# Kernel tuning notes

Hardware: AMD Instinct MI355X
Metric: run time of the kernel (lower is better)

Reference implementation:

```python
import jax, jax.numpy as jnp
import numpy as np

EPS = 1e-5
CHUNK = 512


def _bn(x, gamma, beta):
    # BatchNorm1d in training mode: biased batch statistics over the batch dim
    m = x.mean(axis=0)
    v = ((x - m) ** 2).mean(axis=0)
    return (x - m) * jax.lax.rsqrt(v + EPS) * gamma + beta


def _xavier(k, fan_in, fan_out):
    lim = float(np.sqrt(6.0 / (fan_in + fan_out)))
    return jax.random.uniform(k, (fan_in, fan_out), minval=-lim, maxval=lim, dtype=jnp.float32)


def setup_inputs() -> dict:
    key = jax.random.key(0)
    ks = jax.random.split(key, 10)
    B, CH_S, CH_H, T = 8192, 512, 2048, 3
    D = CH_H * T  # 6144 = 12 chunks of 512
    inp = {
        "fs": jax.random.normal(ks[0], (B, CH_S), dtype=jnp.float32),
        "ft0": jax.random.normal(ks[1], (B, CH_H), dtype=jnp.float32),
        "ft1": jax.random.normal(ks[2], (B, CH_H), dtype=jnp.float32),
        "ft2": jax.random.normal(ks[3], (B, CH_H), dtype=jnp.float32),
        # fixed (non-trainable in the original: plain tensor) score key [512, 1]
        "score_key": jax.random.uniform(ks[4], (CHUNK, 1), dtype=jnp.float32),
        # align_t: Linear(D,2048) -> BN -> Linear(2048,2048) -> BN -> Linear(2048,CH_H) -> ReLU
        "W1": _xavier(ks[5], D, 2048), "b1": jnp.zeros((2048,), jnp.float32),
        "g1": jnp.ones((2048,), jnp.float32), "beta1": jnp.zeros((2048,), jnp.float32),
        "W2": _xavier(ks[6], 2048, 2048), "b2": jnp.zeros((2048,), jnp.float32),
        "g2": jnp.ones((2048,), jnp.float32), "beta2": jnp.zeros((2048,), jnp.float32),
        "W3": _xavier(ks[7], 2048, CH_H), "b3": jnp.zeros((CH_H,), jnp.float32),
        # extend: Linear(CH_H, D) -> ReLU
        "We": _xavier(ks[8], CH_H, D), "bE": jnp.zeros((D,), jnp.float32),
    }
    return inp


def reference(fs, ft0, ft1, ft2, score_key, W1, b1, g1, beta1, W2, b2, g2, beta2, W3, b3, We, bE):
    # fs is accepted but unused, mirroring the original forward
    ft_all = jnp.concatenate([ft0, ft1, ft2], axis=1)  # [B, D]
    B, D = ft_all.shape
    n_chunks = D // CHUNK
    chunks = ft_all.reshape(B, n_chunks, CHUNK)  # [B, C, 512]
    # chunked score matmul against key[512,1], softmax over chunks
    score = jax.nn.softmax(jnp.einsum("bck,k->bc", chunks, score_key[:, 0]), axis=1)  # [B, C]
    # per-chunk reweighting: x <- x + x*score  == x*(1+score), one broadcasted multiply
    ft_all = (chunks * (1.0 + score[:, :, None])).reshape(B, D)
    # align_t MLP (BatchNorm in training mode, no activation between first layers)
    h = _bn(ft_all @ W1 + b1, g1, beta1)
    h = _bn(h @ W2 + b2, g2, beta2)
    aligned_t = jax.nn.relu(h @ W3 + b3)
    extend_t = jax.nn.relu(aligned_t @ We + bE)
    return aligned_t, extend_t, ft_all
```

## Files before the change

kernel.cpp:

```cpp
#include <hip/hip_runtime.h>
#include <hip/hip_bf16.h>
#include <cstdint>
#include <cstddef>

using bf16x8 = __attribute__((ext_vector_type(8))) __bf16;
using f32x4  = __attribute__((ext_vector_type(4))) float;

__device__ __forceinline__ unsigned short f2bf(float f) {
  unsigned int u = __float_as_uint(f);
  u += 0x7FFFu + ((u >> 16) & 1u);
  return (unsigned short)(u >> 16);
}

__device__ __forceinline__ void async_cp16(const void* g, void* l) {
  __builtin_amdgcn_global_load_lds(
      (const __attribute__((address_space(1))) unsigned int*)g,
      (__attribute__((address_space(3))) unsigned int*)l, 16, 0, 0);
}

__global__ __launch_bounds__(256) void wconv(const float* __restrict__ W,
                                             unsigned short* __restrict__ Wt,
                                             int K, int N) {
  __shared__ float tile[32][33];
  const int n0 = blockIdx.x * 32;
  const int k0 = blockIdx.y * 32;
  const int tx = threadIdx.x;
  const int ty = threadIdx.y;
  for (int i = 0; i < 32; i += 8)
    tile[ty + i][tx] = W[(size_t)(k0 + ty + i) * N + n0 + tx];
  __syncthreads();
  for (int i = 0; i < 32; i += 8)
    Wt[(size_t)(n0 + ty + i) * K + k0 + tx] = f2bf(tile[tx][ty + i]);
}

__global__ __launch_bounds__(256) void score_kernel(
    const float* __restrict__ ft0, const float* __restrict__ ft1,
    const float* __restrict__ ft2, const float* __restrict__ key,
    float* __restrict__ out_f, unsigned short* __restrict__ out_b) {
  const int row  = blockIdx.x;
  const int t    = threadIdx.x;
  const int lane = t & 63;
  const int w    = t >> 6;
  const int h    = t >> 7;
  __shared__ float wsum[6][4];
  __shared__ float mult[12];

  const float4* k4 = (const float4*)key;
  float4 v[6];
#pragma unroll
  for (int i = 0; i < 6; i++) {
    const int idx4 = t + 256 * i;
    const int e    = idx4 * 4;
    const float* tsrc = (i < 2) ? ft0 : (i < 4) ? ft1 : ft2;
    v[i] = *(const float4*)(tsrc + (size_t)row * 2048 + (e & 2047));
    float4 kv = k4[idx4 & 127];
    float p = v[i].x * kv.x + v[i].y * kv.y + v[i].z * kv.z + v[i].w * kv.w;
#pragma unroll
    for (int o = 32; o > 0; o >>= 1) p += __shfl_down(p, o, 64);
    if (lane == 0) wsum[i][w] = p;
  }
  __syncthreads();
  if (t == 0) {
    float s[12];
    float mx = -1e30f;
    for (int c = 0; c < 12; c++) {
      s[c] = wsum[c >> 1][2 * (c & 1)] + wsum[c >> 1][2 * (c & 1) + 1];
      mx = fmaxf(mx, s[c]);
    }
    float tot = 0.f;
    for (int c = 0; c < 12; c++) { s[c] = expf(s[c] - mx); tot += s[c]; }
    const float inv = 1.0f / tot;
    for (int c = 0; c < 12; c++) mult[c] = 1.0f + s[c] * inv;
  }
  __syncthreads();
#pragma unroll
  for (int i = 0; i < 6; i++) {
    const int idx4 = t + 256 * i;
    const int e    = idx4 * 4;
    const float m  = mult[2 * i + h];
    float4 o;
    o.x = v[i].x * m; o.y = v[i].y * m; o.z = v[i].z * m; o.w = v[i].w * m;
    *(float4*)(out_f + (size_t)row * 6144 + e) = o;
    ushort4 ob;
    ob.x = f2bf(o.x); ob.y = f2bf(o.y); ob.z = f2bf(o.z); ob.w = f2bf(o.w);
    *(ushort4*)(out_b + (size_t)row * 6144 + e) = ob;
  }
}

template <int EPI>
__global__ __launch_bounds__(256, 2) void gemm_kernel(
    const unsigned short* __restrict__ A,
    const unsigned short* __restrict__ Bt,
    const float* __restrict__ bias,
    float* __restrict__ C,
    unsigned short* __restrict__ Cbf,
    int M, int N, int K) {
  __shared__ __align__(16) unsigned short As[128 * 32];
  __shared__ __align__(16) unsigned short Bs[128 * 32];
  const int t    = threadIdx.x;
  const int lane = t & 63;
  const int w    = t >> 6;
  const size_t m0 = (size_t)blockIdx.y * 128;
  const size_t n0 = (size_t)blockIdx.x * 128;
  const int wm   = (w >> 1) * 64;
  const int wn   = (w & 1) * 64;
  const int frow = lane & 15;
  const int quad = lane >> 4;

  const int c0 = w * 128 + lane;
  const int c1 = c0 + 64;
  const unsigned short* gA0 = A  + (m0 + (c0 >> 2)) * (size_t)K + (c0 & 3) * 8;
  const unsigned short* gA1 = A  + (m0 + (c1 >> 2)) * (size_t)K + (c1 & 3) * 8;
  const unsigned short* gB0 = Bt + (n0 + (c0 >> 2)) * (size_t)K + (c0 & 3) * 8;
  const unsigned short* gB1 = Bt + (n0 + (c1 >> 2)) * (size_t)K + (c1 & 3) * 8;
  unsigned short* lA0 = As + (size_t)(w * 128) * 8;
  unsigned short* lA1 = As + (size_t)(w * 128 + 64) * 8;
  unsigned short* lB0 = Bs + (size_t)(w * 128) * 8;
  unsigned short* lB1 = Bs + (size_t)(w * 128 + 64) * 8;

  f32x4 acc[4][4];
  const f32x4 z = {0.f, 0.f, 0.f, 0.f};
#pragma unroll
  for (int i = 0; i < 4; i++)
#pragma unroll
    for (int j = 0; j < 4; j++) acc[i][j] = z;

  for (int k0 = 0; k0 < K; k0 += 32) {
    async_cp16(gA0 + k0, lA0);
    async_cp16(gA1 + k0, lA1);
    async_cp16(gB0 + k0, lB0);
    async_cp16(gB1 + k0, lB1);
    __syncthreads();
    bf16x8 af[4], bfr[4];
#pragma unroll
    for (int i = 0; i < 4; i++)
      af[i] = *(const bf16x8*)(As + (wm + i * 16 + frow) * 32 + quad * 8);
#pragma unroll
    for (int i = 0; i < 4; i++)
      bfr[i] = *(const bf16x8*)(Bs + (wn + i * 16 + frow) * 32 + quad * 8);
#pragma unroll
    for (int mi = 0; mi < 4; mi++)
#pragma unroll
      for (int ni = 0; ni < 4; ni++)
        acc[mi][ni] = __builtin_amdgcn_mfma_f32_16x16x32_bf16(af[mi], bfr[ni], acc[mi][ni], 0, 0, 0);
    __syncthreads();
  }

#pragma unroll
  for (int mi = 0; mi < 4; mi++) {
    const size_t rowb = m0 + wm + mi * 16 + quad * 4;
#pragma unroll
    for (int ni = 0; ni < 4; ni++) {
      const size_t col = n0 + wn + ni * 16 + frow;
      const float bv = bias[col];
#pragma unroll
      for (int r = 0; r < 4; r++) {
        float v = acc[mi][ni][r] + bv;
        if (EPI == 1) v = fmaxf(v, 0.f);
        const size_t idx = (rowb + r) * (size_t)N + col;
        C[idx] = v;
        if (EPI == 1 && Cbf != nullptr) Cbf[idx] = f2bf(v);
      }
    }
  }
}

__global__ __launch_bounds__(256) void bn_accum(const float* __restrict__ h,
                                                float* __restrict__ ps,
                                                float* __restrict__ pq, int N) {
  const int c  = blockIdx.x * 256 + threadIdx.x;
  const int r0 = blockIdx.y * 256;
  const float* p = h + (size_t)r0 * N + c;
  float s = 0.f, q = 0.f;
  for (int r = 0; r < 256; r++) {
    float x = p[(size_t)r * N];
    s += x; q += x * x;
  }
  ps[(size_t)blockIdx.y * N + c] = s;
  pq[(size_t)blockIdx.y * N + c] = q;
}

__global__ __launch_bounds__(256) void bn_final(const float* __restrict__ ps,
                                                const float* __restrict__ pq,
                                                const float* __restrict__ g,
                                                const float* __restrict__ beta,
                                                float* __restrict__ stats,
                                                int N, int nb, float invM) {
  const int c = blockIdx.x * 256 + threadIdx.x;
  float s = 0.f, q = 0.f;
  for (int b = 0; b < nb; b++) { s += ps[(size_t)b * N + c]; q += pq[(size_t)b * N + c]; }
  const float mean = s * invM;
  const float var  = q * invM - mean * mean;
  const float sc   = g[c] * rsqrtf(var + 1e-5f);
  stats[c]     = sc;
  stats[N + c] = beta[c] - mean * sc;
}

__global__ __launch_bounds__(256) void bn_norm(const float* __restrict__ h,
                                               const float* __restrict__ stats,
                                               unsigned short* __restrict__ hb, int N) {
  const size_t i4 = (size_t)blockIdx.x * 256 + threadIdx.x;
  const float4 x = ((const float4*)h)[i4];
  const int c = (int)((i4 * 4) & (size_t)(N - 1));
  const float4 sc = *(const float4*)(stats + c);
  const float4 tt = *(const float4*)(stats + N + c);
  ushort4 ob;
  ob.x = f2bf(x.x * sc.x + tt.x);
  ob.y = f2bf(x.y * sc.y + tt.y);
  ob.z = f2bf(x.z * sc.z + tt.z);
  ob.w = f2bf(x.w * sc.w + tt.w);
  ((ushort4*)hb)[i4] = ob;
}

extern "C" void kernel_launch(void* const* d_in, const int* in_sizes, int n_in,
                              void* d_out, int out_size, void* d_ws, size_t ws_size,
                              hipStream_t stream) {
  const float* ft0 = (const float*)d_in[1];
  const float* ft1 = (const float*)d_in[2];
  const float* ft2 = (const float*)d_in[3];
  const float* key = (const float*)d_in[4];
  const float* W1  = (const float*)d_in[5];
  const float* b1  = (const float*)d_in[6];
  const float* g1  = (const float*)d_in[7];
  const float* be1 = (const float*)d_in[8];
  const float* W2  = (const float*)d_in[9];
  const float* b2  = (const float*)d_in[10];
  const float* g2  = (const float*)d_in[11];
  const float* be2 = (const float*)d_in[12];
  const float* W3  = (const float*)d_in[13];
  const float* b3  = (const float*)d_in[14];
  const float* We  = (const float*)d_in[15];
  const float* bE  = (const float*)d_in[16];

  float* out         = (float*)d_out;
  float* out_aligned = out;
  float* out_extend  = out + (size_t)8192 * 2048;
  float* out_ft      = out + (size_t)8192 * 2048 + (size_t)8192 * 6144;

  char* ws = (char*)d_ws;
  unsigned short* ft_bf = (unsigned short*)(ws);
  unsigned short* Wt1   = (unsigned short*)(ws + 100663296ull);
  unsigned short* Wt2   = (unsigned short*)(ws + 125829120ull);
  unsigned short* Wt3   = (unsigned short*)(ws + 134217728ull);
  unsigned short* WtE   = (unsigned short*)(ws + 142606336ull);
  float*          hf    = (float*)(ws + 167772160ull);
  unsigned short* hba   = (unsigned short*)(ws + 234881024ull);
  unsigned short* hbb   = (unsigned short*)(ws + 268435456ull);
  float*          psum  = (float*)(ws + 301989888ull);
  float*          psq   = (float*)(ws + 302252032ull);
  float*          stats = (float*)(ws + 302514176ull);

  const dim3 blk32(32, 8);
  wconv<<<dim3(2048 / 32, 6144 / 32), blk32, 0, stream>>>(W1, Wt1, 6144, 2048);
  wconv<<<dim3(2048 / 32, 2048 / 32), blk32, 0, stream>>>(W2, Wt2, 2048, 2048);
  wconv<<<dim3(2048 / 32, 2048 / 32), blk32, 0, stream>>>(W3, Wt3, 2048, 2048);
  wconv<<<dim3(6144 / 32, 2048 / 32), blk32, 0, stream>>>(We, WtE, 2048, 6144);

  score_kernel<<<dim3(8192), dim3(256), 0, stream>>>(ft0, ft1, ft2, key, out_ft, ft_bf);

  gemm_kernel<0><<<dim3(16, 64), dim3(256), 0, stream>>>(ft_bf, Wt1, b1, hf,
                                                         (unsigned short*)nullptr, 8192, 2048, 6144);
  bn_accum<<<dim3(8, 32), dim3(256), 0, stream>>>(hf, psum, psq, 2048);
  bn_final<<<dim3(8), dim3(256), 0, stream>>>(psum, psq, g1, be1, stats, 2048, 32, 1.0f / 8192.0f);
  bn_norm<<<dim3(16384), dim3(256), 0, stream>>>(hf, stats, hba, 2048);

  gemm_kernel<0><<<dim3(16, 64), dim3(256), 0, stream>>>(hba, Wt2, b2, hf,
                                                         (unsigned short*)nullptr, 8192, 2048, 2048);
  bn_accum<<<dim3(8, 32), dim3(256), 0, stream>>>(hf, psum, psq, 2048);
  bn_final<<<dim3(8), dim3(256), 0, stream>>>(psum, psq, g2, be2, stats, 2048, 32, 1.0f / 8192.0f);
  bn_norm<<<dim3(16384), dim3(256), 0, stream>>>(hf, stats, hba, 2048);

  gemm_kernel<1><<<dim3(16, 64), dim3(256), 0, stream>>>(hba, Wt3, b3, out_aligned, hbb,
                                                         8192, 2048, 2048);
  gemm_kernel<1><<<dim3(48, 64), dim3(256), 0, stream>>>(hbb, WtE, bE, out_extend,
                                                         (unsigned short*)nullptr, 8192, 6144, 2048);
}
```

Baseline: 1.464 ms.

## Replace GEMM with 256x256-tile, 4-stage async pipelined, LDS-swizzled kernel

Replaces the 128x128 single-buffered GEMM with a 512-thread kernel that computes 256x256 output tiles. It streams K-slices into a 4-slot LDS ring using async global-to-LDS copies with explicit vmcnt waits, and XOR-swizzles the LDS layout to avoid bank conflicts. It also raises MFMA priority during compute. The aim is to hide global load latency behind compute and raise data reuse per tile. In exchange it uses 128 KB of LDS and many more accumulator registers, which limits occupancy, and the grids become smaller (256 blocks for the square GEMMs).

```diff
diff --git a/kernel.cpp b/kernel.cpp
--- a/kernel.cpp
+++ b/kernel.cpp
@@ -88,74 +88,104 @@
 }
 
 template <int EPI>
-__global__ __launch_bounds__(256, 2) void gemm_kernel(
+__global__ __launch_bounds__(512, 2) void gemm256(
     const unsigned short* __restrict__ A,
     const unsigned short* __restrict__ Bt,
     const float* __restrict__ bias,
     float* __restrict__ C,
     unsigned short* __restrict__ Cbf,
     int M, int N, int K) {
-  __shared__ __align__(16) unsigned short As[128 * 32];
-  __shared__ __align__(16) unsigned short Bs[128 * 32];
+  __shared__ __align__(16) unsigned short smem[65536];
   const int t    = threadIdx.x;
   const int lane = t & 63;
   const int w    = t >> 6;
-  const size_t m0 = (size_t)blockIdx.y * 128;
-  const size_t n0 = (size_t)blockIdx.x * 128;
-  const int wm   = (w >> 1) * 64;
-  const int wn   = (w & 1) * 64;
+  const int wm   = w >> 2;
+  const int wn   = w & 3;
   const int frow = lane & 15;
   const int quad = lane >> 4;
-
-  const int c0 = w * 128 + lane;
-  const int c1 = c0 + 64;
-  const unsigned short* gA0 = A  + (m0 + (c0 >> 2)) * (size_t)K + (c0 & 3) * 8;
-  const unsigned short* gA1 = A  + (m0 + (c1 >> 2)) * (size_t)K + (c1 & 3) * 8;
-  const unsigned short* gB0 = Bt + (n0 + (c0 >> 2)) * (size_t)K + (c0 & 3) * 8;
-  const unsigned short* gB1 = Bt + (n0 + (c1 >> 2)) * (size_t)K + (c1 & 3) * 8;
-  unsigned short* lA0 = As + (size_t)(w * 128) * 8;
-  unsigned short* lA1 = As + (size_t)(w * 128 + 64) * 8;
-  unsigned short* lB0 = Bs + (size_t)(w * 128) * 8;
-  unsigned short* lB1 = Bs + (size_t)(w * 128 + 64) * 8;
-
-  f32x4 acc[4][4];
+  const size_t m0 = (size_t)blockIdx.y * 256;
+  const size_t n0 = (size_t)blockIdx.x * 256;
+
+  const bool isB  = w >= 4;
+  const int  seg  = (w & 3) * 4096;
+  const int  off0 = seg + lane * 16;
+  const int  pos0 = off0 ^ (((off0 >> 7) & 7) << 4);
+  const int  r0   = pos0 >> 6;
+  const int  kb0  = pos0 & 63;
+  const unsigned short* gp =
+      (isB ? Bt + (n0 + (size_t)r0) * K : A + (m0 + (size_t)r0) * K) + (kb0 >> 1);
+  char* lseg = (char*)smem + (isB ? 16384 : 0) + seg;
+
+  const int offA = (wm * 128 + frow) * 64 + quad * 16;
+  const int aoff = offA ^ (((offA >> 7) & 7) << 4);
+  const int offB = (wn * 64 + frow) * 64 + quad * 16;
+  const int boff = 16384 + (offB ^ (((offB >> 7) & 7) << 4));
+
+  f32x4 acc[8][4];
   const f32x4 z = {0.f, 0.f, 0.f, 0.f};
 #pragma unroll
-  for (int i = 0; i < 4; i++)
+  for (int i = 0; i < 8; i++)
 #pragma unroll
     for (int j = 0; j < 4; j++) acc[i][j] = z;
 
-  for (int k0 = 0; k0 < K; k0 += 32) {
-    async_cp16(gA0 + k0, lA0);
-    async_cp16(gA1 + k0, lA1);
-    async_cp16(gB0 + k0, lB0);
-    async_cp16(gB1 + k0, lB1);
-    __syncthreads();
-    bf16x8 af[4], bfr[4];
-#pragma unroll
-    for (int i = 0; i < 4; i++)
-      af[i] = *(const bf16x8*)(As + (wm + i * 16 + frow) * 32 + quad * 8);
-#pragma unroll
-    for (int i = 0; i < 4; i++)
-      bfr[i] = *(const bf16x8*)(Bs + (wn + i * 16 + frow) * 32 + quad * 8);
-#pragma unroll
-    for (int mi = 0; mi < 4; mi++)
-#pragma unroll
-      for (int ni = 0; ni < 4; ni++)
-        acc[mi][ni] = __builtin_amdgcn_mfma_f32_16x16x32_bf16(af[mi], bfr[ni], acc[mi][ni], 0, 0, 0);
-    __syncthreads();
-  }
-
-#pragma unroll
-  for (int mi = 0; mi < 4; mi++) {
-    const size_t rowb = m0 + wm + mi * 16 + quad * 4;
-#pragma unroll
-    for (int ni = 0; ni < 4; ni++) {
-      const size_t col = n0 + wn + ni * 16 + frow;
-      const float bv = bias[col];
-#pragma unroll
-      for (int r = 0; r < 4; r++) {
-        float v = acc[mi][ni][r] + bv;
+  const int nkt = K >> 5;
+
+  auto stage = [&](int slot) {
+    char* lb = lseg + slot * 32768;
+    async_cp16(gp,                  lb);
+    async_cp16(gp + (size_t)16 * K, lb + 1024);
+    async_cp16(gp + (size_t)32 * K, lb + 2048);
+    async_cp16(gp + (size_t)48 * K, lb + 3072);
+    gp += 32;
+  };
+
+  auto compute = [&](int slot) {
+    const char* base = (const char*)smem + slot * 32768;
+    bf16x8 af[8], bv[4];
+#pragma unroll
+    for (int mi = 0; mi < 8; ++mi)
+      af[mi] = *(const bf16x8*)(base + aoff + mi * 1024);
+#pragma unroll
+    for (int ni = 0; ni < 4; ++ni)
+      bv[ni] = *(const bf16x8*)(base + boff + ni * 1024);
+    __builtin_amdgcn_s_setprio(1);
+#pragma unroll
+    for (int mi = 0; mi < 8; ++mi)
+#pragma unroll
+      for (int ni = 0; ni < 4; ++ni)
+        acc[mi][ni] = __builtin_amdgcn_mfma_f32_16x16x32_bf16(af[mi], bv[ni], acc[mi][ni], 0, 0, 0);
+    __builtin_amdgcn_s_setprio(0);
+  };
+
+  stage(0); stage(1); stage(2);
+  int kt = 0;
+  for (; kt + 3 < nkt; ++kt) {
+    stage((kt + 3) & 3);
+    asm volatile("s_waitcnt vmcnt(12)" ::: "memory");
+    asm volatile("s_barrier" ::: "memory");
+    compute(kt & 3);
+    asm volatile("s_waitcnt lgkmcnt(0)\n\ts_barrier" ::: "memory");
+  }
+  asm volatile("s_waitcnt vmcnt(8)" ::: "memory");
+  asm volatile("s_barrier" ::: "memory");
+  compute(kt & 3); ++kt;
+  asm volatile("s_waitcnt vmcnt(4)" ::: "memory");
+  asm volatile("s_barrier" ::: "memory");
+  compute(kt & 3); ++kt;
+  asm volatile("s_waitcnt vmcnt(0)" ::: "memory");
+  asm volatile("s_barrier" ::: "memory");
+  compute(kt & 3);
+
+#pragma unroll
+  for (int mi = 0; mi < 8; ++mi) {
+    const size_t rowb = m0 + wm * 128 + mi * 16 + quad * 4;
+#pragma unroll
+    for (int ni = 0; ni < 4; ++ni) {
+      const size_t col = n0 + wn * 64 + ni * 16 + frow;
+      const float bvs = bias[col];
+#pragma unroll
+      for (int r = 0; r < 4; ++r) {
+        float v = acc[mi][ni][r] + bvs;
         if (EPI == 1) v = fmaxf(v, 0.f);
         const size_t idx = (rowb + r) * (size_t)N + col;
         C[idx] = v;
@@ -258,20 +288,20 @@
 
   score_kernel<<<dim3(8192), dim3(256), 0, stream>>>(ft0, ft1, ft2, key, out_ft, ft_bf);
 
-  gemm_kernel<0><<<dim3(16, 64), dim3(256), 0, stream>>>(ft_bf, Wt1, b1, hf,
-                                                         (unsigned short*)nullptr, 8192, 2048, 6144);
+  gemm256<0><<<dim3(8, 32), dim3(512), 0, stream>>>(ft_bf, Wt1, b1, hf,
+                                                    (unsigned short*)nullptr, 8192, 2048, 6144);
   bn_accum<<<dim3(8, 32), dim3(256), 0, stream>>>(hf, psum, psq, 2048);
   bn_final<<<dim3(8), dim3(256), 0, stream>>>(psum, psq, g1, be1, stats, 2048, 32, 1.0f / 8192.0f);
   bn_norm<<<dim3(16384), dim3(256), 0, stream>>>(hf, stats, hba, 2048);
 
-  gemm_kernel<0><<<dim3(16, 64), dim3(256), 0, stream>>>(hba, Wt2, b2, hf,
-                                                         (unsigned short*)nullptr, 8192, 2048, 2048);
+  gemm256<0><<<dim3(8, 32), dim3(512), 0, stream>>>(hba, Wt2, b2, hf,
+                                                    (unsigned short*)nullptr, 8192, 2048, 2048);
   bn_accum<<<dim3(8, 32), dim3(256), 0, stream>>>(hf, psum, psq, 2048);
   bn_final<<<dim3(8), dim3(256), 0, stream>>>(psum, psq, g2, be2, stats, 2048, 32, 1.0f / 8192.0f);
   bn_norm<<<dim3(16384), dim3(256), 0, stream>>>(hf, stats, hba, 2048);
 
-  gemm_kernel<1><<<dim3(16, 64), dim3(256), 0, stream>>>(hba, Wt3, b3, out_aligned, hbb,
-                                                         8192, 2048, 2048);
-  gemm_kernel<1><<<dim3(48, 64), dim3(256), 0, stream>>>(hbb, WtE, bE, out_extend,
-                                                         (unsigned short*)nullptr, 8192, 6144, 2048);
-}
+  gemm256<1><<<dim3(8, 32), dim3(512), 0, stream>>>(hba, Wt3, b3, out_aligned, hbb,
+                                                    8192, 2048, 2048);
+  gemm256<1><<<dim3(24, 32), dim3(512), 0, stream>>>(hbb, WtE, bE, out_extend,
+                                                     (unsigned short*)nullptr, 8192, 6144, 2048);
+}
```

Result: faster. 1.384 ms (-5.5%).
